# Kernel tuning notes

Hardware: AMD Instinct MI355X
Metric: run time of the kernel (lower is better)

## Reference

```python
import jax, jax.numpy as jnp
import numpy as np

NUM_GRAPHS = 256
BN_EPS = 1e-5


def _bn(x, g, b, m, v):
    # eval-mode BatchNorm1d: affine with running stats
    return (x - m) * jax.lax.rsqrt(v + BN_EPS) * g + b


def setup_inputs() -> dict:
    key = jax.random.key(0)
    ks = jax.random.split(key, 16)
    N = 500_000
    x = jax.random.normal(ks[0], (N, 3), dtype=jnp.float32)
    batch = jnp.sort(jax.random.randint(ks[1], (N,), 0, NUM_GRAPHS, dtype=jnp.int32))

    def lin(k, fan_in, fan_out):
        kw, kb = jax.random.split(k)
        s = 1.0 / np.sqrt(fan_in)
        W = jax.random.uniform(kw, (fan_in, fan_out), jnp.float32, -s, s)
        b = jax.random.uniform(kb, (fan_out,), jnp.float32, -s, s)
        return W, b

    def bn_params(k, dim):
        k1, k2, k3, k4 = jax.random.split(k, 4)
        g = 1.0 + 0.05 * jax.random.normal(k1, (dim,), jnp.float32)
        be = 0.05 * jax.random.normal(k2, (dim,), jnp.float32)
        m = 0.05 * jax.random.normal(k3, (dim,), jnp.float32)
        v = 0.5 + jax.random.uniform(k4, (dim,), jnp.float32)
        return g, be, m, v

    W1, b1 = lin(ks[2], 3, 64)
    g1, be1, m1, v1 = bn_params(ks[3], 64)
    W2, b2 = lin(ks[4], 64, 64)          # plain last layer of local MLP
    W3, b3 = lin(ks[5], 64, 128)
    g3, be3, m3, v3 = bn_params(ks[6], 128)
    W4, b4 = lin(ks[7], 128, 1024)       # plain last layer of global MLP

    return {
        "x": x, "batch": batch,
        "W1": W1, "b1": b1, "g1": g1, "be1": be1, "m1": m1, "v1": v1,
        "W2": W2, "b2": b2,
        "W3": W3, "b3": b3, "g3": g3, "be3": be3, "m3": m3, "v3": v3,
        "W4": W4, "b4": b4,
    }


def reference(x, batch, W1, b1, g1, be1, m1, v1, W2, b2,
              W3, b3, g3, be3, m3, v3, W4, b4):
    # local MLP [3, 64, 64]: Linear->BN->ReLU, plain last
    h = jax.nn.relu(_bn(x @ W1 + b1, g1, be1, m1, v1))   # [N, 64]
    h = h @ W2 + b2                                       # [N, 64]
    # global MLP [64, 128, 1024]: Linear->BN->ReLU, plain last
    h = jax.nn.relu(_bn(h @ W3 + b3, g3, be3, m3, v3))    # [N, 128]
    h = h @ W4 + b4                                       # [N, 1024]
    # global_max_pool: ragged scatter-max over per-point graph ids
    out = jax.ops.segment_max(h, batch, num_segments=NUM_GRAPHS)  # [G, 1024]
    return out
```

## Files before the change

kernel.cpp:

```cpp
#include <hip/hip_runtime.h>
#include <hip/hip_bf16.h>
#include <cstdint>

typedef __attribute__((ext_vector_type(8))) short bf16x8;
typedef __attribute__((ext_vector_type(4))) float f32x4;

#define BN_EPS 1e-5f

__device__ __forceinline__ unsigned short f2bf(float f) {
    unsigned int u = __float_as_uint(f);
    unsigned int r = (u + 0x7FFFu + ((u >> 16) & 1u)) >> 16;
    return (unsigned short)r;
}
__device__ __forceinline__ float bf2f(unsigned short h) {
    return __uint_as_float(((unsigned int)h) << 16);
}
__device__ __forceinline__ unsigned int encf(float f) {
    unsigned int u = __float_as_uint(f);
    return (u & 0x80000000u) ? ~u : (u | 0x80000000u);
}
__device__ __forceinline__ float decf(unsigned int e) {
    return __uint_as_float((e & 0x80000000u) ? (e & 0x7FFFFFFFu) : ~e);
}

__device__ __forceinline__ long long lbound(const int* __restrict__ b, long long n, int key) {
    long long lo = 0, hi = n;
    while (lo < hi) { long long mid = (lo + hi) >> 1; if (b[mid] < key) lo = mid + 1; else hi = mid; }
    return lo;
}

__device__ __forceinline__ void gl_lds16(const unsigned short* g, unsigned short* l) {
    __builtin_amdgcn_global_load_lds((const __attribute__((address_space(1))) unsigned int*)g,
                                     (__attribute__((address_space(3))) unsigned int*)l,
                                     16, 0, 0);
}

__global__ void fold_kernel(const float* __restrict__ W1, const float* __restrict__ b1,
                            const float* __restrict__ g1, const float* __restrict__ be1,
                            const float* __restrict__ m1, const float* __restrict__ v1,
                            const float* __restrict__ W2, const float* __restrict__ b2,
                            const float* __restrict__ W3, const float* __restrict__ b3,
                            const float* __restrict__ g3, const float* __restrict__ be3,
                            const float* __restrict__ m3, const float* __restrict__ v3,
                            const float* __restrict__ W4,
                            unsigned short* __restrict__ W4p,
                            unsigned short* __restrict__ W23ph, unsigned short* __restrict__ W23pl,
                            float* __restrict__ W1c, float* __restrict__ b23,
                            unsigned int* __restrict__ out, int out_size) {
    int tid = blockIdx.x * blockDim.x + threadIdx.x;
    if (tid < 131072) {
        int j = tid & 7, lane = (tid >> 3) & 63, kf = (tid >> 9) & 3, nt = tid >> 11;
        int col = nt * 16 + (lane & 15);
        int k = kf * 32 + (lane >> 4) * 8 + j;
        W4p[tid] = f2bf(W4[k * 1024 + col]);
    }
    if (tid < out_size) out[tid] = 0x007FFFFFu;
    if (tid + 131072 < out_size) out[tid + 131072] = 0x007FFFFFu;
    if (tid < 8192) {
        int j = tid & 7, lane = (tid >> 3) & 63, kf = (tid >> 9) & 1, nn = tid >> 10;
        int col = nn * 16 + (lane & 15);
        int k = kf * 32 + (lane >> 4) * 8 + j;
        float s3 = g3[col] / sqrtf(v3[col] + BN_EPS);
        float acc = 0.f;
        for (int o = 0; o < 64; ++o) acc += W2[k * 64 + o] * W3[o * 128 + col];
        float w = acc * s3;
        unsigned short hi = f2bf(w);
        W23ph[tid] = hi;
        W23pl[tid] = f2bf(w - bf2f(hi));
    }
    if (tid < 128) {
        float s3 = g3[tid] / sqrtf(v3[tid] + BN_EPS);
        float acc = b3[tid] - m3[tid];
        for (int o = 0; o < 64; ++o) acc += b2[o] * W3[o * 128 + tid];
        b23[tid] = acc * s3 + be3[tid];
    }
    if (tid < 256) {
        int o = tid >> 2, c = tid & 3;
        float s1 = g1[o] / sqrtf(v1[o] + BN_EPS);
        W1c[tid] = (c < 3) ? W1[c * 64 + o] * s1 : (b1[o] - m1[o]) * s1 + be1[o];
    }
}

__global__ __launch_bounds__(128, 4) void fused_kernel(const float* __restrict__ x,
                                                       const float* __restrict__ W1c,
                                                       const unsigned short* __restrict__ W23ph,
                                                       const unsigned short* __restrict__ W23pl,
                                                       const float* __restrict__ b23,
                                                       const unsigned short* __restrict__ W4p,
                                                       const float* __restrict__ b4,
                                                       const int* __restrict__ batch,
                                                       unsigned int* __restrict__ out,
                                                       float* __restrict__ tilemax,
                                                       int* __restrict__ gtile,
                                                       long long pbase, int ntiles, long long Ntot) {
    __shared__ unsigned short ldss[2][8192];
    int wave = blockIdx.x * 2 + (threadIdx.x >> 6);
    if (wave >= ntiles) return;
    unsigned short* h3 = ldss[threadIdx.x >> 6];
    int lane = threadIdx.x & 63;
    int q = lane >> 4, r16 = lane & 15;
    long long p0 = pbase + (long long)wave * 64;

    float xv[4][3];
    bool valid[4];
#pragma unroll
    for (int mt = 0; mt < 4; ++mt) {
        long long p = p0 + mt * 16 + r16;
        if (p < Ntot) {
            xv[mt][0] = x[p * 3 + 0]; xv[mt][1] = x[p * 3 + 1]; xv[mt][2] = x[p * 3 + 2];
            valid[mt] = true;
        } else {
            xv[mt][0] = xv[mt][1] = xv[mt][2] = 0.f; valid[mt] = false;
        }
    }
    bf16x8 a2[4][2];
#pragma unroll
    for (int kf = 0; kf < 2; ++kf)
#pragma unroll
        for (int j = 0; j < 8; ++j) {
            int f = kf * 32 + q * 8 + j;
            float4 w = *reinterpret_cast<const float4*>(W1c + f * 4);
#pragma unroll
            for (int mt = 0; mt < 4; ++mt) {
                float v = fmaf(xv[mt][0], w.x, fmaf(xv[mt][1], w.y, fmaf(xv[mt][2], w.z, w.w)));
                v = valid[mt] ? fmaxf(v, 0.f) : 0.f;
                a2[mt][kf][j] = (short)f2bf(v);
            }
        }

    bf16x8 a[4][4];
#pragma unroll
    for (int half = 0; half < 2; ++half) {
#pragma unroll
        for (int n = 0; n < 4; ++n) {
            int nn = half * 4 + n;
            f32x4 acc2[4];
#pragma unroll
            for (int mt = 0; mt < 4; ++mt) acc2[mt] = (f32x4){0.f, 0.f, 0.f, 0.f};
#pragma unroll
            for (int kf = 0; kf < 2; ++kf) {
                bf16x8 bh = *reinterpret_cast<const bf16x8*>(W23ph + (size_t)((nn * 2 + kf) * 64 + lane) * 8);
                bf16x8 bl = *reinterpret_cast<const bf16x8*>(W23pl + (size_t)((nn * 2 + kf) * 64 + lane) * 8);
#pragma unroll
                for (int mt = 0; mt < 4; ++mt) {
                    acc2[mt] = __builtin_amdgcn_mfma_f32_16x16x32_bf16(a2[mt][kf], bh, acc2[mt], 0, 0, 0);
                    acc2[mt] = __builtin_amdgcn_mfma_f32_16x16x32_bf16(a2[mt][kf], bl, acc2[mt], 0, 0, 0);
                }
            }
            int col = nn * 16 + r16;
            float bias = b23[col];
#pragma unroll
            for (int mt = 0; mt < 4; ++mt)
#pragma unroll
                for (int r = 0; r < 4; ++r) {
                    int row = mt * 16 + q * 4 + r;
                    float v = fmaxf(acc2[mt][r] + bias, 0.f);
                    h3[row * 72 + n * 16 + r16] = f2bf(v);
                }
        }
        asm volatile("s_waitcnt lgkmcnt(0)" ::: "memory");
#pragma unroll
        for (int mt = 0; mt < 4; ++mt)
#pragma unroll
            for (int kfl = 0; kfl < 2; ++kfl)
                a[mt][half * 2 + kfl] =
                    *reinterpret_cast<const bf16x8*>(h3 + (16 * mt + r16) * 72 + kfl * 32 + q * 8);
        asm volatile("s_waitcnt lgkmcnt(0)" ::: "memory");
    }

    long long plast = p0 + 63; if (plast > Ntot - 1) plast = Ntot - 1;
    int gfirst = batch[(p0 < Ntot) ? p0 : (Ntot - 1)];
    int glast = batch[plast];
    bool fast = (gfirst == glast) && (p0 + 63 < Ntot);
    if (lane == 0) gtile[wave] = fast ? gfirst : -1;

    if (fast) {
        float* tmlds = (float*)(h3 + 6144);
#pragma unroll
        for (int t = 0; t < 3; ++t)
#pragma unroll
            for (int kf = 0; kf < 4; ++kf)
                gl_lds16(W4p + (size_t)((t * 4 + kf) * 512) + lane * 8,
                         h3 + t * 2048 + kf * 512);
        unsigned lbase = (unsigned)(size_t)(__attribute__((address_space(3))) unsigned short*)h3;
        unsigned laddr0 = lbase + (unsigned)lane * 16u;

        int s = 0;
        for (int g8 = 0; g8 < 8; ++g8) {
            float m8[8];
#pragma unroll
            for (int i8 = 0; i8 < 8; ++i8) {
                int nt = g8 * 8 + i8;
                unsigned ad = laddr0 + (unsigned)s * 4096u;
                bf16x8 b0, b1, b2, b3;
                asm volatile("s_waitcnt vmcnt(8)\n\t"
                             "ds_read_b128 %0, %4 offset:0\n\t"
                             "ds_read_b128 %1, %4 offset:1024\n\t"
                             "ds_read_b128 %2, %4 offset:2048\n\t"
                             "ds_read_b128 %3, %4 offset:3072\n\t"
                             "s_waitcnt lgkmcnt(0)"
                             : "=&v"(b0), "=&v"(b1), "=&v"(b2), "=&v"(b3)
                             : "v"(ad) : "memory");
                f32x4 acc[4];
#pragma unroll
                for (int mt = 0; mt < 4; ++mt) acc[mt] = (f32x4){0.f, 0.f, 0.f, 0.f};
#pragma unroll
                for (int mt = 0; mt < 4; ++mt) {
                    acc[mt] = __builtin_amdgcn_mfma_f32_16x16x32_bf16(a[mt][0], b0, acc[mt], 0, 0, 0);
                    acc[mt] = __builtin_amdgcn_mfma_f32_16x16x32_bf16(a[mt][1], b1, acc[mt], 0, 0, 0);
                    acc[mt] = __builtin_amdgcn_mfma_f32_16x16x32_bf16(a[mt][2], b2, acc[mt], 0, 0, 0);
                    acc[mt] = __builtin_amdgcn_mfma_f32_16x16x32_bf16(a[mt][3], b3, acc[mt], 0, 0, 0);
                }
                {
                    int ntn = (nt + 3) & 63;
#pragma unroll
                    for (int kf = 0; kf < 4; ++kf)
                        gl_lds16(W4p + (size_t)((ntn * 4 + kf) * 512) + lane * 8,
                                 h3 + s * 2048 + kf * 512);
                }
                s = (s == 2) ? 0 : s + 1;
                float m = fmaxf(fmaxf(fmaxf(acc[0][0], acc[0][1]), fmaxf(acc[0][2], acc[0][3])),
                                fmaxf(fmaxf(acc[1][0], acc[1][1]), fmaxf(acc[1][2], acc[1][3])));
                m = fmaxf(m, fmaxf(fmaxf(fmaxf(acc[2][0], acc[2][1]), fmaxf(acc[2][2], acc[2][3])),
                                   fmaxf(fmaxf(acc[3][0], acc[3][1]), fmaxf(acc[3][2], acc[3][3]))));
                m8[i8] = m;
            }
#pragma unroll
            for (int qq = 0; qq < 8; ++qq) {
                float v = m8[qq];
                v = fmaxf(v, __shfl_xor(v, 16));
                v = fmaxf(v, __shfl_xor(v, 32));
                m8[qq] = v;
            }
            if (lane < 16) {
#pragma unroll
                for (int qq = 0; qq < 8; ++qq) tmlds[(g8 * 8 + qq) * 16 + lane] = m8[qq];
            }
        }
        asm volatile("s_waitcnt vmcnt(0) lgkmcnt(0)" ::: "memory");
        float* tm = tilemax + (size_t)wave * 1024;
#pragma unroll
        for (int t = 0; t < 4; ++t) {
            f32x4 v = *reinterpret_cast<const f32x4*>(tmlds + t * 256 + lane * 4);
            *reinterpret_cast<f32x4*>(tm + t * 256 + lane * 4) = v;
        }
        return;
    }

    int gl = -1;
    unsigned long long smask = 0;
    int grow[16];
    {
        long long pl = p0 + lane;
        gl = (pl < Ntot) ? batch[pl] : -1;
        int gprev = __shfl_up(gl, 1);
        bool is_start = (lane == 0) || (gl != gprev);
        smask = __ballot(is_start);
#pragma unroll
        for (int m = 0; m < 4; ++m)
#pragma unroll
            for (int r = 0; r < 4; ++r) {
                int rw = m * 16 + (lane >> 4) * 4 + r;
                grow[m * 4 + r] = __shfl(gl, rw);
            }
    }

    for (int nt = 0; nt < 64; ++nt) {
        bf16x8 bq[4];
#pragma unroll
        for (int kf = 0; kf < 4; ++kf)
            bq[kf] = *reinterpret_cast<const bf16x8*>(W4p + (size_t)((nt * 4 + kf) * 64 + lane) * 8);
        f32x4 acc[4];
#pragma unroll
        for (int m = 0; m < 4; ++m) acc[m] = (f32x4){0.f, 0.f, 0.f, 0.f};
#pragma unroll
        for (int kf = 0; kf < 4; ++kf)
#pragma unroll
            for (int m = 0; m < 4; ++m)
                acc[m] = __builtin_amdgcn_mfma_f32_16x16x32_bf16(a[m][kf], bq[kf], acc[m], 0, 0, 0);

        int col = nt * 16 + (lane & 15);
        float bias = b4[col];
        unsigned long long tmp = smask;
        while (tmp) {
            int ls = __builtin_ctzll(tmp); tmp &= tmp - 1;
            int gs = __shfl(gl, ls);
            float m = -INFINITY;
#pragma unroll
            for (int mm = 0; mm < 4; ++mm)
#pragma unroll
                for (int r = 0; r < 4; ++r)
                    if (grow[mm * 4 + r] == gs) m = fmaxf(m, acc[mm][r]);
            m = fmaxf(m, __shfl_xor(m, 16));
            m = fmaxf(m, __shfl_xor(m, 32));
            if (gs >= 0 && lane < 16 && m > -INFINITY)
                atomicMax(&out[gs * 1024 + col], encf(m + bias));
        }
    }
}

__global__ __launch_bounds__(256) void reduce_chunk(const float* __restrict__ tilemax,
                                                    const int* __restrict__ gtile,
                                                    const int* __restrict__ batch,
                                                    const float* __restrict__ b4,
                                                    unsigned int* __restrict__ out,
                                                    long long base, long long npts, long long N,
                                                    int finalize) {
    int g = blockIdx.x >> 2;
    int col = (blockIdx.x & 3) * 256 + threadIdx.x;
    __shared__ int sh[2];
    if (threadIdx.x == 0) {
        long long lo = lbound(batch, N, g);
        long long hi = lbound(batch, N, g + 1);
        long long e = base + npts;
        if (lo < base) lo = base;
        if (hi > e) hi = e;
        sh[0] = (int)(lo - base);
        sh[1] = (int)(hi - base);
    }
    __syncthreads();
    int lo = sh[0], hi = sh[1];
    if (!finalize && lo >= hi) return;
    float m = -INFINITY;
    if (lo < hi) {
        int t0 = lo >> 6, t1 = (hi - 1) >> 6;
        for (int t = t0; t <= t1; ++t)
            if (gtile[t] == g) m = fmaxf(m, tilemax[(size_t)t * 1024 + col]);
    }
    int idx = g * 1024 + col;
    if (finalize) {
        float cur = decf(out[idx]);
        if (m > -INFINITY) cur = fmaxf(cur, m + b4[col]);
        out[idx] = __float_as_uint(cur);
    } else {
        if (m > -INFINITY) atomicMax(&out[idx], encf(m + b4[col]));
    }
}

extern "C" void kernel_launch(void* const* d_in, const int* in_sizes, int n_in,
                              void* d_out, int out_size, void* d_ws, size_t ws_size,
                              hipStream_t stream) {
    const float* x   = (const float*)d_in[0];
    const int* batch = (const int*)d_in[1];
    const float* W1  = (const float*)d_in[2];
    const float* b1  = (const float*)d_in[3];
    const float* g1  = (const float*)d_in[4];
    const float* be1 = (const float*)d_in[5];
    const float* m1  = (const float*)d_in[6];
    const float* v1  = (const float*)d_in[7];
    const float* W2  = (const float*)d_in[8];
    const float* b2  = (const float*)d_in[9];
    const float* W3  = (const float*)d_in[10];
    const float* b3  = (const float*)d_in[11];
    const float* g3  = (const float*)d_in[12];
    const float* be3 = (const float*)d_in[13];
    const float* m3  = (const float*)d_in[14];
    const float* v3  = (const float*)d_in[15];
    const float* W4  = (const float*)d_in[16];
    const float* b4  = (const float*)d_in[17];

    long long N = in_sizes[1];

    char* ws = (char*)d_ws;
    unsigned short* W4p   = (unsigned short*)(ws + 0);
    unsigned short* W23ph = (unsigned short*)(ws + 262144);
    unsigned short* W23pl = (unsigned short*)(ws + 278528);
    float* W1c = (float*)(ws + 294912);
    float* b23 = (float*)(ws + 295936);

    fold_kernel<<<512, 256, 0, stream>>>(W1, b1, g1, be1, m1, v1, W2, b2, W3, b3, g3, be3, m3, v3,
                                         W4, W4p, W23ph, W23pl, W1c, b23,
                                         (unsigned int*)d_out, out_size);

    const size_t ofs = 1 << 20;
    size_t avail = (ws_size > ofs) ? ws_size - ofs : 0;
    long long Tcap = (long long)(avail / 4104);
    Tcap &= ~3LL;
    if (Tcap < 4) Tcap = 4;
    long long ntiles_tot = (N + 63) / 64;
    long long ntcap = (ntiles_tot + 3) & ~3LL;
    if (Tcap > ntcap) Tcap = ntcap;

    float* tilemax = (float*)(ws + ofs);
    int* gtile = (int*)(ws + ofs + (size_t)Tcap * 4096);
    long long chunk = Tcap * 64;

    for (long long base = 0; base < N; base += chunk) {
        long long npts = N - base; if (npts > chunk) npts = chunk;
        int ntiles = (int)((npts + 63) / 64);
        int blocks = (ntiles + 1) / 2;
        fused_kernel<<<blocks, 128, 0, stream>>>(x, W1c, W23ph, W23pl, b23, W4p, b4, batch,
                                                 (unsigned int*)d_out, tilemax, gtile,
                                                 base, ntiles, N);
        int finalize = (base + chunk >= N) ? 1 : 0;
        reduce_chunk<<<1024, 256, 0, stream>>>(tilemax, gtile, batch, b4, (unsigned int*)d_out,
                                               base, npts, N, finalize);
    }
}
```

Baseline: 248.5 us.

## Share W4 LDS ring across four waves with barrier-synchronized cooperative loads

Blocks grow from two to four waves. All waves now share one triple-buffered LDS ring for W4 tiles instead of each wave streaming its own copy. Each wave loads one quarter of every tile, and block barriers guard reuse of the ring, so W4 traffic and LDS footprint per wave drop. The fast and slow (multi-graph) paths are merged into one loop, and the fast path writes tile maxima straight to global memory instead of staging them in LDS. In exchange, every wave now hits two barriers per column tile, inactive waves have to stay in the loop, and the slow path also stalls at those barriers.

```diff
diff --git a/kernel.cpp b/kernel.cpp
--- a/kernel.cpp
+++ b/kernel.cpp
@@ -81,7 +81,7 @@
     }
 }
 
-__global__ __launch_bounds__(128, 4) void fused_kernel(const float* __restrict__ x,
+__global__ __launch_bounds__(256, 3) void fused_kernel(const float* __restrict__ x,
                                                        const float* __restrict__ W1c,
                                                        const unsigned short* __restrict__ W23ph,
                                                        const unsigned short* __restrict__ W23pl,
@@ -93,11 +93,13 @@
                                                        float* __restrict__ tilemax,
                                                        int* __restrict__ gtile,
                                                        long long pbase, int ntiles, long long Ntot) {
-    __shared__ unsigned short ldss[2][8192];
-    int wave = blockIdx.x * 2 + (threadIdx.x >> 6);
-    if (wave >= ntiles) return;
-    unsigned short* h3 = ldss[threadIdx.x >> 6];
+    __shared__ unsigned short ldsall[24576];
+    int wv = threadIdx.x >> 6;
     int lane = threadIdx.x & 63;
+    int wave = blockIdx.x * 4 + wv;
+    bool active = wave < ntiles;
+    unsigned short* h3 = ldsall + wv * 4608;
+    unsigned short* ring = ldsall + 18432;
     int q = lane >> 4, r16 = lane & 15;
     long long p0 = pbase + (long long)wave * 64;
 
@@ -106,7 +108,7 @@
 #pragma unroll
     for (int mt = 0; mt < 4; ++mt) {
         long long p = p0 + mt * 16 + r16;
-        if (p < Ntot) {
+        if (active && p < Ntot) {
             xv[mt][0] = x[p * 3 + 0]; xv[mt][1] = x[p * 3 + 1]; xv[mt][2] = x[p * 3 + 2];
             valid[mt] = true;
         } else {
@@ -168,63 +170,107 @@
         asm volatile("s_waitcnt lgkmcnt(0)" ::: "memory");
     }
 
-    long long plast = p0 + 63; if (plast > Ntot - 1) plast = Ntot - 1;
-    int gfirst = batch[(p0 < Ntot) ? p0 : (Ntot - 1)];
-    int glast = batch[plast];
-    bool fast = (gfirst == glast) && (p0 + 63 < Ntot);
-    if (lane == 0) gtile[wave] = fast ? gfirst : -1;
-
-    if (fast) {
-        float* tmlds = (float*)(h3 + 6144);
-#pragma unroll
-        for (int t = 0; t < 3; ++t)
-#pragma unroll
-            for (int kf = 0; kf < 4; ++kf)
-                gl_lds16(W4p + (size_t)((t * 4 + kf) * 512) + lane * 8,
-                         h3 + t * 2048 + kf * 512);
-        unsigned lbase = (unsigned)(size_t)(__attribute__((address_space(3))) unsigned short*)h3;
-        unsigned laddr0 = lbase + (unsigned)lane * 16u;
-
-        int s = 0;
-        for (int g8 = 0; g8 < 8; ++g8) {
-            float m8[8];
-#pragma unroll
-            for (int i8 = 0; i8 < 8; ++i8) {
-                int nt = g8 * 8 + i8;
-                unsigned ad = laddr0 + (unsigned)s * 4096u;
-                bf16x8 b0, b1, b2, b3;
-                asm volatile("s_waitcnt vmcnt(8)\n\t"
-                             "ds_read_b128 %0, %4 offset:0\n\t"
-                             "ds_read_b128 %1, %4 offset:1024\n\t"
-                             "ds_read_b128 %2, %4 offset:2048\n\t"
-                             "ds_read_b128 %3, %4 offset:3072\n\t"
-                             "s_waitcnt lgkmcnt(0)"
-                             : "=&v"(b0), "=&v"(b1), "=&v"(b2), "=&v"(b3)
-                             : "v"(ad) : "memory");
-                f32x4 acc[4];
-#pragma unroll
-                for (int mt = 0; mt < 4; ++mt) acc[mt] = (f32x4){0.f, 0.f, 0.f, 0.f};
-#pragma unroll
-                for (int mt = 0; mt < 4; ++mt) {
-                    acc[mt] = __builtin_amdgcn_mfma_f32_16x16x32_bf16(a[mt][0], b0, acc[mt], 0, 0, 0);
-                    acc[mt] = __builtin_amdgcn_mfma_f32_16x16x32_bf16(a[mt][1], b1, acc[mt], 0, 0, 0);
-                    acc[mt] = __builtin_amdgcn_mfma_f32_16x16x32_bf16(a[mt][2], b2, acc[mt], 0, 0, 0);
-                    acc[mt] = __builtin_amdgcn_mfma_f32_16x16x32_bf16(a[mt][3], b3, acc[mt], 0, 0, 0);
-                }
-                {
-                    int ntn = (nt + 3) & 63;
-#pragma unroll
-                    for (int kf = 0; kf < 4; ++kf)
-                        gl_lds16(W4p + (size_t)((ntn * 4 + kf) * 512) + lane * 8,
-                                 h3 + s * 2048 + kf * 512);
-                }
-                s = (s == 2) ? 0 : s + 1;
+    bool fast = false;
+    int gl = -1;
+    unsigned long long smask = 0;
+    if (active) {
+        long long plast = p0 + 63; if (plast > Ntot - 1) plast = Ntot - 1;
+        int gfirst = batch[(p0 < Ntot) ? p0 : (Ntot - 1)];
+        int glast = batch[plast];
+        fast = (gfirst == glast) && (p0 + 63 < Ntot);
+        if (lane == 0) gtile[wave] = fast ? gfirst : -1;
+        if (!fast) {
+            long long pl = p0 + lane;
+            gl = (pl < Ntot) ? batch[pl] : -1;
+            int gprev = __shfl_up(gl, 1);
+            smask = __ballot((lane == 0) || (gl != gprev));
+        }
+    }
+    int grow[16];
+    if (active && !fast) {
+#pragma unroll
+        for (int m = 0; m < 4; ++m)
+#pragma unroll
+            for (int r = 0; r < 4; ++r)
+                grow[m * 4 + r] = __shfl(gl, m * 16 + (lane >> 4) * 4 + r);
+    }
+
+    float* tm = tilemax + (size_t)wave * 1024;
+
+#pragma unroll
+    for (int t = 0; t < 3; ++t)
+        gl_lds16(W4p + (size_t)((t * 4 + wv) * 512) + lane * 8,
+                 ring + t * 2048 + wv * 512);
+    unsigned ringb = (unsigned)(size_t)(__attribute__((address_space(3))) unsigned short*)ring;
+    unsigned laddr = ringb + (unsigned)lane * 16u;
+
+    int s = 0;
+    for (int g8 = 0; g8 < 8; ++g8) {
+        float m8[8];
+#pragma unroll
+        for (int i8 = 0; i8 < 8; ++i8) {
+            int nt = g8 * 8 + i8;
+            if (i8 >= 3) {
+                asm volatile("s_waitcnt vmcnt(2)" ::: "memory");
+            } else if (g8 == 0) {
+                asm volatile("s_waitcnt vmcnt(2)" ::: "memory");
+            } else {
+                asm volatile("s_waitcnt vmcnt(10)" ::: "memory");
+            }
+            __builtin_amdgcn_s_barrier();
+            unsigned ad = laddr + (unsigned)s * 4096u;
+            bf16x8 b0, b1, b2, b3;
+            asm volatile("ds_read_b128 %0, %4 offset:0\n\t"
+                         "ds_read_b128 %1, %4 offset:1024\n\t"
+                         "ds_read_b128 %2, %4 offset:2048\n\t"
+                         "ds_read_b128 %3, %4 offset:3072\n\t"
+                         "s_waitcnt lgkmcnt(0)"
+                         : "=&v"(b0), "=&v"(b1), "=&v"(b2), "=&v"(b3)
+                         : "v"(ad) : "memory");
+            __builtin_amdgcn_s_barrier();
+            {
+                int ntn = (nt + 3) & 63;
+                gl_lds16(W4p + (size_t)((ntn * 4 + wv) * 512) + lane * 8,
+                         ring + s * 2048 + wv * 512);
+            }
+            s = (s == 2) ? 0 : s + 1;
+            f32x4 acc[4];
+#pragma unroll
+            for (int mt = 0; mt < 4; ++mt) acc[mt] = (f32x4){0.f, 0.f, 0.f, 0.f};
+#pragma unroll
+            for (int mt = 0; mt < 4; ++mt) {
+                acc[mt] = __builtin_amdgcn_mfma_f32_16x16x32_bf16(a[mt][0], b0, acc[mt], 0, 0, 0);
+                acc[mt] = __builtin_amdgcn_mfma_f32_16x16x32_bf16(a[mt][1], b1, acc[mt], 0, 0, 0);
+                acc[mt] = __builtin_amdgcn_mfma_f32_16x16x32_bf16(a[mt][2], b2, acc[mt], 0, 0, 0);
+                acc[mt] = __builtin_amdgcn_mfma_f32_16x16x32_bf16(a[mt][3], b3, acc[mt], 0, 0, 0);
+            }
+            if (fast) {
                 float m = fmaxf(fmaxf(fmaxf(acc[0][0], acc[0][1]), fmaxf(acc[0][2], acc[0][3])),
                                 fmaxf(fmaxf(acc[1][0], acc[1][1]), fmaxf(acc[1][2], acc[1][3])));
                 m = fmaxf(m, fmaxf(fmaxf(fmaxf(acc[2][0], acc[2][1]), fmaxf(acc[2][2], acc[2][3])),
                                    fmaxf(fmaxf(acc[3][0], acc[3][1]), fmaxf(acc[3][2], acc[3][3]))));
                 m8[i8] = m;
-            }
+            } else if (active) {
+                int col = nt * 16 + (lane & 15);
+                float bias = b4[col];
+                unsigned long long tmp = smask;
+                while (tmp) {
+                    int ls = __builtin_ctzll(tmp); tmp &= tmp - 1;
+                    int gs = __shfl(gl, ls);
+                    float m = -INFINITY;
+#pragma unroll
+                    for (int mm = 0; mm < 4; ++mm)
+#pragma unroll
+                        for (int r = 0; r < 4; ++r)
+                            if (grow[mm * 4 + r] == gs) m = fmaxf(m, acc[mm][r]);
+                    m = fmaxf(m, __shfl_xor(m, 16));
+                    m = fmaxf(m, __shfl_xor(m, 32));
+                    if (gs >= 0 && lane < 16 && m > -INFINITY)
+                        atomicMax(&out[gs * 1024 + col], encf(m + bias));
+                }
+            }
+        }
+        if (fast) {
 #pragma unroll
             for (int qq = 0; qq < 8; ++qq) {
                 float v = m8[qq];
@@ -234,67 +280,8 @@
             }
             if (lane < 16) {
 #pragma unroll
-                for (int qq = 0; qq < 8; ++qq) tmlds[(g8 * 8 + qq) * 16 + lane] = m8[qq];
-            }
-        }
-        asm volatile("s_waitcnt vmcnt(0) lgkmcnt(0)" ::: "memory");
-        float* tm = tilemax + (size_t)wave * 1024;
-#pragma unroll
-        for (int t = 0; t < 4; ++t) {
-            f32x4 v = *reinterpret_cast<const f32x4*>(tmlds + t * 256 + lane * 4);
-            *reinterpret_cast<f32x4*>(tm + t * 256 + lane * 4) = v;
-        }
-        return;
-    }
-
-    int gl = -1;
-    unsigned long long smask = 0;
-    int grow[16];
-    {
-        long long pl = p0 + lane;
-        gl = (pl < Ntot) ? batch[pl] : -1;
-        int gprev = __shfl_up(gl, 1);
-        bool is_start = (lane == 0) || (gl != gprev);
-        smask = __ballot(is_start);
-#pragma unroll
-        for (int m = 0; m < 4; ++m)
-#pragma unroll
-            for (int r = 0; r < 4; ++r) {
-                int rw = m * 16 + (lane >> 4) * 4 + r;
-                grow[m * 4 + r] = __shfl(gl, rw);
-            }
-    }
-
-    for (int nt = 0; nt < 64; ++nt) {
-        bf16x8 bq[4];
-#pragma unroll
-        for (int kf = 0; kf < 4; ++kf)
-            bq[kf] = *reinterpret_cast<const bf16x8*>(W4p + (size_t)((nt * 4 + kf) * 64 + lane) * 8);
-        f32x4 acc[4];
-#pragma unroll
-        for (int m = 0; m < 4; ++m) acc[m] = (f32x4){0.f, 0.f, 0.f, 0.f};
-#pragma unroll
-        for (int kf = 0; kf < 4; ++kf)
-#pragma unroll
-            for (int m = 0; m < 4; ++m)
-                acc[m] = __builtin_amdgcn_mfma_f32_16x16x32_bf16(a[m][kf], bq[kf], acc[m], 0, 0, 0);
-
-        int col = nt * 16 + (lane & 15);
-        float bias = b4[col];
-        unsigned long long tmp = smask;
-        while (tmp) {
-            int ls = __builtin_ctzll(tmp); tmp &= tmp - 1;
-            int gs = __shfl(gl, ls);
-            float m = -INFINITY;
-#pragma unroll
-            for (int mm = 0; mm < 4; ++mm)
-#pragma unroll
-                for (int r = 0; r < 4; ++r)
-                    if (grow[mm * 4 + r] == gs) m = fmaxf(m, acc[mm][r]);
-            m = fmaxf(m, __shfl_xor(m, 16));
-            m = fmaxf(m, __shfl_xor(m, 32));
-            if (gs >= 0 && lane < 16 && m > -INFINITY)
-                atomicMax(&out[gs * 1024 + col], encf(m + bias));
+                for (int qq = 0; qq < 8; ++qq) tm[(g8 * 8 + qq) * 16 + lane] = m8[qq];
+            }
         }
     }
 }
@@ -388,8 +375,8 @@
     for (long long base = 0; base < N; base += chunk) {
         long long npts = N - base; if (npts > chunk) npts = chunk;
         int ntiles = (int)((npts + 63) / 64);
-        int blocks = (ntiles + 1) / 2;
-        fused_kernel<<<blocks, 128, 0, stream>>>(x, W1c, W23ph, W23pl, b23, W4p, b4, batch,
+        int blocks = (ntiles + 3) / 4;
+        fused_kernel<<<blocks, 256, 0, stream>>>(x, W1c, W23ph, W23pl, b23, W4p, b4, batch,
                                                  (unsigned int*)d_out, tilemax, gtile,
                                                  base, ntiles, N);
         int finalize = (base + chunk >= N) ? 1 : 0;
```

Measured after the change: 210.7 us. 1.18x faster.
